# Performance work log

Measured on AMD Instinct MI355X. Metric: run time of the kernel, lower is better.

The kernel has to match this reference:

```python
import jax, jax.numpy as jnp
import numpy as np

ALPHA = 0.2  # LeakyReLU negative slope
NEG_INF = -9e15

def setup_inputs() -> dict:
    key = jax.random.key(0)
    k1, k2, k3, k4, k5 = jax.random.split(key, 5)
    B, N, Fin, Fout = 8, 2048, 128, 128
    h = jax.random.normal(k1, (B, N, Fin), dtype=jnp.float32)
    adj = jax.random.randint(k2, (N, N), 0, 2, dtype=jnp.int32)
    dist = jax.random.uniform(k3, (N, N), dtype=jnp.float32)
    W = jax.random.normal(k4, (Fin, Fout), dtype=jnp.float32) * (1.414 * (6.0 / (Fin + Fout)) ** 0.5)
    a = jax.random.normal(k5, (2 * Fout, 1), dtype=jnp.float32) * 0.1
    distance_scaler = jnp.ones((1,), dtype=jnp.float32)
    return {"h": h, "adj": adj, "dist": dist, "W": W, "a": a, "distance_scaler": distance_scaler}

def reference(h, adj, dist, W, a, distance_scaler):
    # h: [B,N,Fin], adj/dist: [N,N], W: [Fin,Fout], a: [2*Fout,1]
    h_prime = jnp.einsum('bnf,fh->bnh', h, W)              # [B,N,Fout]
    Fout = h_prime.shape[-1]
    a1, a2 = a[:Fout, 0], a[Fout:, 0]
    # additive score: a1.h_i + a2.h_j, equivalent to cat([h_i,h_j]) @ a
    si = h_prime @ a1                                      # [B,N]
    sj = h_prime @ a2                                      # [B,N]
    e = jax.nn.leaky_relu(si[:, :, None] + sj[:, None, :], negative_slope=ALPHA)  # [B,N,N]
    dist_bias = -jnp.log(dist + 1e-6) * distance_scaler[0]  # [N,N]
    scores = e + dist_bias[None, :, :]
    scores = jnp.where(adj[None, :, :] > 0, scores, NEG_INF)
    attention = jax.nn.softmax(scores, axis=2)             # [B,N,N]
    # dropout=identity in eval mode
    out = jnp.einsum('bij,bjh->bih', attention, h_prime)   # [B,N,Fout]
    return jax.nn.elu(out)
```

## Files before the change

kernel.cpp:

```cpp
#include <hip/hip_runtime.h>
#include <hip/hip_bf16.h>

typedef __attribute__((ext_vector_type(4))) float f32x4;
typedef __attribute__((ext_vector_type(8))) short short8;
typedef __attribute__((ext_vector_type(4))) unsigned short ushort4v;
typedef _Float16 f16x8 __attribute__((ext_vector_type(8)));

#define NB 8
#define NN 2048
#define NF 128
#define LOG2E 1.4426950408889634f
#define MASK_NEG_H -60000.0f

static __device__ __forceinline__ unsigned short f2bf(float f) {
    union { __hip_bfloat16 b; unsigned short u; } cv;
    cv.b = __float2bfloat16(f);
    return cv.u;
}

static __device__ __forceinline__ void gload_lds16(const void* g, void* l) {
    __builtin_amdgcn_global_load_lds(
        (const __attribute__((address_space(1))) unsigned int*)g,
        (__attribute__((address_space(3))) unsigned int*)l, 16, 0, 0);
}

__global__ __launch_bounds__(256) void k_pre(
    const float* __restrict__ h, const int* __restrict__ adj,
    const float* __restrict__ dist, const float* __restrict__ W,
    const float* __restrict__ a, const float* __restrict__ scaler,
    unsigned short* __restrict__ vfrag, float* __restrict__ siC,
    float* __restrict__ sjC, _Float16* __restrict__ biasF)
{
    __shared__ __align__(16) unsigned char smem[34816];
    const int bid = blockIdx.x;
    const int t = threadIdx.x;

    if (bid < 256) {
        unsigned char* WT = smem;
        float* wa1 = (float*)(smem + 32768);
        float* wa2 = wa1 + NF;

        const int lane = t & 63;
        const int w = t >> 6;
        const int b = bid >> 5;
        const int i0 = (bid & 31) << 6;

        {
            const int f = t >> 1;
            const int c0 = (t & 1) << 6;
            float s1 = 0.f, s2 = 0.f;
            const float* wrow = W + f * NF + c0;
            const float* a1p = a + c0;
            const float* a2p = a + NF + c0;
            #pragma unroll 8
            for (int c = 0; c < 64; ++c) {
                float wv = wrow[c];
                s1 += wv * a1p[c];
                s2 += wv * a2p[c];
                int col = c0 + c;
                int dst = col * 256 + ((2 * f) ^ ((col & 15) << 4));
                *reinterpret_cast<unsigned short*>(&WT[dst]) = f2bf(wv);
            }
            s1 += __shfl_xor(s1, 1);
            s2 += __shfl_xor(s2, 1);
            if ((t & 1) == 0) { wa1[f] = s1 * LOG2E; wa2[f] = s2 * LOG2E; }
        }
        __syncthreads();

        const int l15 = lane & 15;
        const int arow = i0 + w * 16 + l15;
        const int kofs = (lane >> 4) << 3;
        const float* hrow = h + (size_t)(b * NN + arow) * NF + kofs;
        const int swz = l15 << 4;

        f32x4 acc[8];
        #pragma unroll
        for (int nt = 0; nt < 8; ++nt) acc[nt] = (f32x4)(0.f);
        float s1 = 0.f, s2 = 0.f;

        #pragma unroll
        for (int k0 = 0; k0 < NF; k0 += 32) {
            f32x4 h0 = *reinterpret_cast<const f32x4*>(hrow + k0);
            f32x4 h1 = *reinterpret_cast<const f32x4*>(hrow + k0 + 4);
            f32x4 w1lo = *reinterpret_cast<const f32x4*>(&wa1[k0 + kofs]);
            f32x4 w1hi = *reinterpret_cast<const f32x4*>(&wa1[k0 + kofs + 4]);
            f32x4 w2lo = *reinterpret_cast<const f32x4*>(&wa2[k0 + kofs]);
            f32x4 w2hi = *reinterpret_cast<const f32x4*>(&wa2[k0 + kofs + 4]);
            short8 af;
            #pragma unroll
            for (int e = 0; e < 4; ++e) {
                s1 += h0[e] * w1lo[e] + h1[e] * w1hi[e];
                s2 += h0[e] * w2lo[e] + h1[e] * w2hi[e];
                af[e]     = (short)f2bf(h0[e]);
                af[4 + e] = (short)f2bf(h1[e]);
            }
            const int ib = (2 * (k0 + kofs)) ^ swz;
            #pragma unroll
            for (int nt = 0; nt < 8; ++nt) {
                short8 bf8 = *reinterpret_cast<short8*>(&WT[(nt * 16 + l15) * 256 + ib]);
                acc[nt] = __builtin_amdgcn_mfma_f32_16x16x32_bf16(af, bf8, acc[nt], 0, 0, 0);
            }
        }

        s1 += __shfl_xor(s1, 16); s1 += __shfl_xor(s1, 32);
        s2 += __shfl_xor(s2, 16); s2 += __shfl_xor(s2, 32);
        if (lane < 16) {
            siC[b * NN + arow] = s1;
            sjC[b * NN + arow] = s2;
        }

        const int J0 = i0 + w * 16 + ((lane >> 4) << 2);
        const int s = J0 >> 5;
        const int jq = (J0 >> 3) & 3;
        const int eh = J0 & 7;
        #pragma unroll
        for (int nt = 0; nt < 8; ++nt) {
            ushort4v pk;
            #pragma unroll
            for (int e = 0; e < 4; ++e) pk[e] = f2bf(acc[nt][e]);
            *reinterpret_cast<ushort4v*>(
                vfrag + (((size_t)(b * 64 + s) * 8 + nt) * 64 + (l15 | (jq << 4))) * 8 + eh) = pk;
        }
    } else {
        _Float16 (*st)[64][8] = (_Float16 (*)[64][8])smem;
        const int bid2 = bid - 256;
        const int iblk = bid2 >> 3;
        const int jch = bid2 & 7;
        const int i_l = t >> 4;
        const int o2 = t & 15;
        const int i = iblk * 16 + i_l;
        const int jbase = jch * 256 + o2 * 16;
        const float sc = scaler[0];

        const int* ap = adj + (size_t)i * NN + jbase;
        const float* dp = dist + (size_t)i * NN + jbase;
        int av[16]; float dv[16];
        *reinterpret_cast<int4*>(&av[0])  = *reinterpret_cast<const int4*>(ap);
        *reinterpret_cast<int4*>(&av[4])  = *reinterpret_cast<const int4*>(ap + 4);
        *reinterpret_cast<int4*>(&av[8])  = *reinterpret_cast<const int4*>(ap + 8);
        *reinterpret_cast<int4*>(&av[12]) = *reinterpret_cast<const int4*>(ap + 12);
        *reinterpret_cast<float4*>(&dv[0])  = *reinterpret_cast<const float4*>(dp);
        *reinterpret_cast<float4*>(&dv[4])  = *reinterpret_cast<const float4*>(dp + 4);
        *reinterpret_cast<float4*>(&dv[8])  = *reinterpret_cast<const float4*>(dp + 8);
        *reinterpret_cast<float4*>(&dv[12]) = *reinterpret_cast<const float4*>(dp + 12);

        #pragma unroll
        for (int u = 0; u < 2; ++u) {
            const int sl = (o2 * 2 + u) >> 2;
            const int jq = (o2 * 2 + u) & 3;
            f16x8 pk;
            #pragma unroll
            for (int e = 0; e < 8; ++e) {
                const int idx = u * 8 + e;
                float v = (av[idx] > 0) ? (-__log2f(dv[idx] + 1e-6f) * sc) : MASK_NEG_H;
                pk[e] = (_Float16)v;
            }
            *reinterpret_cast<f16x8*>(&st[sl][i_l | (jq << 4)][0]) = pk;
        }
        __syncthreads();

        const int w = t >> 6, lane = t & 63;
        #pragma unroll
        for (int sub = 0; sub < 2; ++sub) {
            const int fs = w * 2 + sub;
            *reinterpret_cast<f16x8*>(
                biasF + ((size_t)(iblk * 64 + jch * 8 + fs) * 64 + lane) * 8) =
                *reinterpret_cast<f16x8*>(&st[fs][lane][0]);
        }
    }
}

__global__ __launch_bounds__(512) void k_attn(
    const unsigned short* __restrict__ vfrag, const float* __restrict__ siC,
    const float* __restrict__ sjC, const _Float16* __restrict__ biasF,
    float* __restrict__ out)
{
    __shared__ __align__(16) unsigned char vbuf[3][32768];
    __shared__ float lp[2][4][16];

    const int t = threadIdx.x;
    const int lane = t & 63;
    const int w = t >> 6;
    const int rt = w & 3;
    const int jh = w >> 2;
    const int l15 = lane & 15;
    const int hi = lane >> 4;

    const int b = blockIdx.x & 7;
    const int rg = blockIdx.x >> 3;

    const int rowbase = rg * 64 + rt * 16;
    const float si0 = siC[b * NN + rowbase + l15];

    const unsigned short* vsrc = vfrag + (size_t)b * 262144 + w * 512 + lane * 8;
    const int ldst = w * 1024;

    const _Float16* bp = biasF + ((size_t)((rg * 4 + rt) * 64) * 64 + lane) * 8;
    const float* sjb = sjC + b * NN + hi * 8;

    f32x4 acc[8];
    #pragma unroll
    for (int ct = 0; ct < 8; ++ct) acc[ct] = (f32x4)(0.f);
    float ls0 = 0.f;

#define STAGE(TL, BUF)                                                        \
    { const unsigned short* gs = vsrc + (TL) * 16384;                         \
      unsigned char* lb = &vbuf[BUF][ldst];                                   \
      gload_lds16(gs,         lb);                                            \
      gload_lds16(gs + 4096,  lb + 8192);                                     \
      gload_lds16(gs + 8192,  lb + 16384);                                    \
      gload_lds16(gs + 12288, lb + 24576); }

    f32x4 sjA0, sjA1, sjB0, sjB1;
    f16x8 bvA, bvB;

#define PREFETCH_SB(TL)                                                       \
    { const int sA = (TL) * 4 + jh * 2;                                       \
      sjA0 = *reinterpret_cast<const f32x4*>(sjb + sA * 32);                  \
      sjA1 = *reinterpret_cast<const f32x4*>(sjb + sA * 32 + 4);              \
      bvA  = *reinterpret_cast<const f16x8*>(bp + sA * 512);                  \
      sjB0 = *reinterpret_cast<const f32x4*>(sjb + sA * 32 + 32);             \
      sjB1 = *reinterpret_cast<const f32x4*>(sjb + sA * 32 + 36);             \
      bvB  = *reinterpret_cast<const f16x8*>(bp + sA * 512 + 512); }

#define QSTEP(SJ0, SJ1, BV, LSL, BUF)                                         \
    { short8 pa;                                                              \
      _Pragma("unroll")                                                       \
      for (int e = 0; e < 8; ++e) {                                           \
          const float sjv = (e < 4) ? SJ0[e] : SJ1[e - 4];                    \
          float x = si0 + sjv;                                                \
          x = fmaxf(x, 0.2f * x) + (float)BV[e];                              \
          float p = __builtin_amdgcn_exp2f(x);                                \
          ls0 += p;                                                           \
          pa[e] = (short)f2bf(p);                                             \
      }                                                                       \
      _Pragma("unroll")                                                       \
      for (int ct = 0; ct < 8; ++ct) {                                        \
          const short8 bfr = *reinterpret_cast<const short8*>(                \
              &vbuf[BUF][((LSL) * 8 + ct) * 1024 + lane * 16]);               \
          acc[ct] = __builtin_amdgcn_mfma_f32_16x16x32_bf16(pa, bfr, acc[ct], 0, 0, 0); \
      } }

    STAGE(0, 0)
    PREFETCH_SB(0)
    STAGE(1, 1)

    for (int tl = 0; tl < 15; ++tl) {
        const int buf = tl % 3;
        asm volatile("s_waitcnt vmcnt(10)" ::: "memory");
        __builtin_amdgcn_s_barrier();
        QSTEP(sjA0, sjA1, bvA, jh * 2, buf)
        QSTEP(sjB0, sjB1, bvB, jh * 2 + 1, buf)
        PREFETCH_SB(tl + 1)
        if (tl + 2 < 16) STAGE(tl + 2, (tl + 2) % 3)
        __builtin_amdgcn_s_barrier();
    }
    {
        asm volatile("s_waitcnt vmcnt(6)" ::: "memory");
        __builtin_amdgcn_s_barrier();
        QSTEP(sjA0, sjA1, bvA, jh * 2, 0)
        QSTEP(sjB0, sjB1, bvB, jh * 2 + 1, 0)
    }
#undef STAGE
#undef PREFETCH_SB
#undef QSTEP

    ls0 += __shfl_xor(ls0, 16);
    ls0 += __shfl_xor(ls0, 32);
    if (lane < 16) lp[jh][rt][l15] = ls0;
    __syncthreads();

    if (jh == 1) {
        #pragma unroll
        for (int ct = 0; ct < 8; ++ct)
            *reinterpret_cast<f32x4*>(&vbuf[1][(rt * 8 + ct) * 1024 + lane * 16]) = acc[ct];
    }
    __syncthreads();
    if (jh == 0) {
        float linv[4];
        #pragma unroll
        for (int e = 0; e < 4; ++e) {
            const int rr = (hi << 2) + e;
            linv[e] = 1.0f / (lp[0][rt][rr] + lp[1][rt][rr]);
        }
        #pragma unroll
        for (int ct = 0; ct < 8; ++ct) {
            f32x4 o = acc[ct] + *reinterpret_cast<const f32x4*>(
                &vbuf[1][(rt * 8 + ct) * 1024 + lane * 16]);
            const int col = ct * 16 + l15;
            #pragma unroll
            for (int e = 0; e < 4; ++e) {
                const int row = rowbase + (hi << 2) + e;
                float v = o[e] * linv[e];
                v = (v > 0.f) ? v : expm1f(v);
                out[(size_t)(b * NN + row) * NF + col] = v;
            }
        }
    }
}

extern "C" void kernel_launch(void* const* d_in, const int* in_sizes, int n_in,
                              void* d_out, int out_size, void* d_ws, size_t ws_size,
                              hipStream_t stream) {
    (void)in_sizes; (void)n_in; (void)out_size; (void)ws_size;
    const float* h      = (const float*)d_in[0];
    const int*   adj    = (const int*)d_in[1];
    const float* dist   = (const float*)d_in[2];
    const float* W      = (const float*)d_in[3];
    const float* a      = (const float*)d_in[4];
    const float* scaler = (const float*)d_in[5];
    float* out = (float*)d_out;

    char* ws = (char*)d_ws;
    unsigned short* vfrag = (unsigned short*)ws;
    float* siC      = (float*)(ws + 4 * 1024 * 1024);
    float* sjC      = (float*)(ws + 4 * 1024 * 1024 + 65536);
    _Float16* biasF = (_Float16*)(ws + 4 * 1024 * 1024 + 2 * 65536);

    k_pre<<<dim3(1280), dim3(256), 0, stream>>>(h, adj, dist, W, a, scaler,
                                                vfrag, siC, sjC, biasF);
    k_attn<<<dim3(NB * NN / 64), dim3(512), 0, stream>>>(vfrag, siC, sjC, biasF, out);
}
```

Measured before the change: 43.45 us.

## Deepen attention pipeline to four smaller stages and stage bias through LDS

The j-loop now runs as 32 half-size tiles in a 4-deep LDS ring instead of 16 tiles in a 3-deep ring. Each stage loads V and the fp16 bias tile into LDS with async global-to-LDS loads, so bias no longer goes through per-thread register prefetches. The loop also drops one barrier per iteration, and the MFMA section is wrapped in s_setprio to favour matrix issue. The intent is more loads in flight and less exposed memory latency, at the cost of more, smaller iterations with a barrier each and a changed LDS footprint for the final reduction.

```diff
diff --git a/kernel.cpp b/kernel.cpp
--- a/kernel.cpp
+++ b/kernel.cpp
@@ -175,7 +175,7 @@
     const float* __restrict__ sjC, const _Float16* __restrict__ biasF,
     float* __restrict__ out)
 {
-    __shared__ __align__(16) unsigned char vbuf[3][32768];
+    __shared__ __align__(16) unsigned char vbuf[4][24576];
     __shared__ float lp[2][4][16];
 
     const int t = threadIdx.x;
@@ -192,77 +192,75 @@
     const int rowbase = rg * 64 + rt * 16;
     const float si0 = siC[b * NN + rowbase + l15];
 
-    const unsigned short* vsrc = vfrag + (size_t)b * 262144 + w * 512 + lane * 8;
-    const int ldst = w * 1024;
-
-    const _Float16* bp = biasF + ((size_t)((rg * 4 + rt) * 64) * 64 + lane) * 8;
     const float* sjb = sjC + b * NN + hi * 8;
+    const unsigned short* vsrcb = vfrag + (size_t)b * 262144 + w * 512 + lane * 8;
+    const _Float16* bsrcb = biasF + ((size_t)((rg * 4 + (w & 3)) * 64) * 64 + lane) * 8;
 
     f32x4 acc[8];
     #pragma unroll
     for (int ct = 0; ct < 8; ++ct) acc[ct] = (f32x4)(0.f);
     float ls0 = 0.f;
-
-#define STAGE(TL, BUF)                                                        \
-    { const unsigned short* gs = vsrc + (TL) * 16384;                         \
-      unsigned char* lb = &vbuf[BUF][ldst];                                   \
-      gload_lds16(gs,         lb);                                            \
-      gload_lds16(gs + 4096,  lb + 8192);                                     \
-      gload_lds16(gs + 8192,  lb + 16384);                                    \
-      gload_lds16(gs + 12288, lb + 24576); }
-
-    f32x4 sjA0, sjA1, sjB0, sjB1;
-    f16x8 bvA, bvB;
-
-#define PREFETCH_SB(TL)                                                       \
-    { const int sA = (TL) * 4 + jh * 2;                                       \
+    f32x4 sjA0, sjA1;
+
+#define STAGE(TL)                                                             \
+    { unsigned char* lb = &vbuf[(TL) & 3][w * 1024];                          \
+      const unsigned short* gsV = vsrcb + (TL) * 8192;                        \
+      gload_lds16(gsV,        lb);                                            \
+      gload_lds16(gsV + 4096, lb + 8192);                                     \
+      gload_lds16(bsrcb + (size_t)(2 * (TL) + (w >> 2)) * 512,                \
+                  &vbuf[(TL) & 3][16384 + w * 1024]); }
+
+#define PF_SJ(TL)                                                             \
+    { const int sA = 2 * (TL) + jh;                                           \
       sjA0 = *reinterpret_cast<const f32x4*>(sjb + sA * 32);                  \
-      sjA1 = *reinterpret_cast<const f32x4*>(sjb + sA * 32 + 4);              \
-      bvA  = *reinterpret_cast<const f16x8*>(bp + sA * 512);                  \
-      sjB0 = *reinterpret_cast<const f32x4*>(sjb + sA * 32 + 32);             \
-      sjB1 = *reinterpret_cast<const f32x4*>(sjb + sA * 32 + 36);             \
-      bvB  = *reinterpret_cast<const f16x8*>(bp + sA * 512 + 512); }
-
-#define QSTEP(SJ0, SJ1, BV, LSL, BUF)                                         \
-    { short8 pa;                                                              \
+      sjA1 = *reinterpret_cast<const f32x4*>(sjb + sA * 32 + 4); }
+
+#define QSTEP(BUF)                                                            \
+    { const f16x8 bv = *reinterpret_cast<const f16x8*>(                       \
+          &vbuf[BUF][16384 + (jh * 4 + rt) * 1024 + lane * 16]);              \
+      short8 pa;                                                              \
       _Pragma("unroll")                                                       \
       for (int e = 0; e < 8; ++e) {                                           \
-          const float sjv = (e < 4) ? SJ0[e] : SJ1[e - 4];                    \
+          const float sjv = (e < 4) ? sjA0[e] : sjA1[e - 4];                  \
           float x = si0 + sjv;                                                \
-          x = fmaxf(x, 0.2f * x) + (float)BV[e];                              \
+          x = fmaxf(x, 0.2f * x) + (float)bv[e];                              \
           float p = __builtin_amdgcn_exp2f(x);                                \
           ls0 += p;                                                           \
           pa[e] = (short)f2bf(p);                                             \
       }                                                                       \
+      __builtin_amdgcn_s_setprio(1);                                          \
       _Pragma("unroll")                                                       \
       for (int ct = 0; ct < 8; ++ct) {                                        \
           const short8 bfr = *reinterpret_cast<const short8*>(                \
-              &vbuf[BUF][((LSL) * 8 + ct) * 1024 + lane * 16]);               \
+              &vbuf[BUF][jh * 8192 + ct * 1024 + lane * 16]);                 \
           acc[ct] = __builtin_amdgcn_mfma_f32_16x16x32_bf16(pa, bfr, acc[ct], 0, 0, 0); \
-      } }
-
-    STAGE(0, 0)
-    PREFETCH_SB(0)
-    STAGE(1, 1)
-
-    for (int tl = 0; tl < 15; ++tl) {
-        const int buf = tl % 3;
-        asm volatile("s_waitcnt vmcnt(10)" ::: "memory");
+      }                                                                       \
+      __builtin_amdgcn_s_setprio(0); }
+
+    STAGE(0)
+    PF_SJ(0)
+    asm volatile("" ::: "memory");
+    STAGE(1)
+    STAGE(2)
+
+    for (int tl = 0; tl < 30; ++tl) {
+        asm volatile("s_waitcnt vmcnt(3)" ::: "memory");
         __builtin_amdgcn_s_barrier();
-        QSTEP(sjA0, sjA1, bvA, jh * 2, buf)
-        QSTEP(sjB0, sjB1, bvB, jh * 2 + 1, buf)
-        PREFETCH_SB(tl + 1)
-        if (tl + 2 < 16) STAGE(tl + 2, (tl + 2) % 3)
-        __builtin_amdgcn_s_barrier();
+        QSTEP(tl & 3)
+        PF_SJ(tl + 1)
+        asm volatile("" ::: "memory");
+        if (tl < 29) STAGE(tl + 3)
     }
-    {
-        asm volatile("s_waitcnt vmcnt(6)" ::: "memory");
-        __builtin_amdgcn_s_barrier();
-        QSTEP(sjA0, sjA1, bvA, jh * 2, 0)
-        QSTEP(sjB0, sjB1, bvB, jh * 2 + 1, 0)
-    }
+    asm volatile("s_waitcnt vmcnt(3)" ::: "memory");
+    __builtin_amdgcn_s_barrier();
+    QSTEP(2)
+    PF_SJ(31)
+    asm volatile("s_waitcnt vmcnt(0)" ::: "memory");
+    __builtin_amdgcn_s_barrier();
+    QSTEP(3)
+
 #undef STAGE
-#undef PREFETCH_SB
+#undef PF_SJ
 #undef QSTEP
 
     ls0 += __shfl_xor(ls0, 16);
@@ -273,7 +271,9 @@
     if (jh == 1) {
         #pragma unroll
         for (int ct = 0; ct < 8; ++ct)
-            *reinterpret_cast<f32x4*>(&vbuf[1][(rt * 8 + ct) * 1024 + lane * 16]) = acc[ct];
+            *reinterpret_cast<f32x4*>(
+                &vbuf[0][((rt * 8 + ct) * 64 + lane) * 16 % 24576 +
+                         (((rt * 8 + ct) * 64 + lane) * 16 / 24576) * 24576]) = acc[ct];
     }
     __syncthreads();
     if (jh == 0) {
@@ -285,8 +285,9 @@
         }
         #pragma unroll
         for (int ct = 0; ct < 8; ++ct) {
+            const int off = ((rt * 8 + ct) * 64 + lane) * 16;
             f32x4 o = acc[ct] + *reinterpret_cast<const f32x4*>(
-                &vbuf[1][(rt * 8 + ct) * 1024 + lane * 16]);
+                &vbuf[0][off % 24576 + (off / 24576) * 24576]);
             const int col = ct * 16 + l15;
             #pragma unroll
             for (int e = 0; e < 4; ++e) {
```

After: 49.52 us. +14.0%, slower.

## Factor exponentials out of attention scores and drop the per-tile trailing barrier

Applied to the files above, without the earlier changes.

Rewrites exp2(leaky(si+sj)+bias) as max(2^si*2^sj, 2^(0.2si)*2^(0.2sj)) * 2^bias, so the exponentials are computed once per node and once per adjacency entry in the prep kernel. The inner loop then needs only multiplies and a max instead of an exp per score. The bias is stored as a bf16 multiplier, with zero for masked edges. It also removes the second barrier per tile, raises wave priority around the MFMA section, and adjusts the vmcnt waits. The risks are overflow or underflow of the factored exponentials, since there is no max subtraction, and a possible LDS race now that the trailing barrier is gone.

```diff
diff --git a/kernel.cpp b/kernel.cpp
--- a/kernel.cpp
+++ b/kernel.cpp
@@ -3,19 +3,22 @@
 
 typedef __attribute__((ext_vector_type(4))) float f32x4;
 typedef __attribute__((ext_vector_type(8))) short short8;
+typedef __attribute__((ext_vector_type(8))) unsigned short ushort8;
 typedef __attribute__((ext_vector_type(4))) unsigned short ushort4v;
-typedef _Float16 f16x8 __attribute__((ext_vector_type(8)));
 
 #define NB 8
 #define NN 2048
 #define NF 128
 #define LOG2E 1.4426950408889634f
-#define MASK_NEG_H -60000.0f
 
 static __device__ __forceinline__ unsigned short f2bf(float f) {
     union { __hip_bfloat16 b; unsigned short u; } cv;
     cv.b = __float2bfloat16(f);
     return cv.u;
+}
+
+static __device__ __forceinline__ float bf2f(unsigned short u) {
+    return __uint_as_float(((unsigned int)u) << 16);
 }
 
 static __device__ __forceinline__ void gload_lds16(const void* g, void* l) {
@@ -29,7 +32,8 @@
     const float* __restrict__ dist, const float* __restrict__ W,
     const float* __restrict__ a, const float* __restrict__ scaler,
     unsigned short* __restrict__ vfrag, float* __restrict__ siC,
-    float* __restrict__ sjC, _Float16* __restrict__ biasF)
+    float* __restrict__ EJ, float* __restrict__ FJ,
+    unsigned short* __restrict__ biasF)
 {
     __shared__ __align__(16) unsigned char smem[34816];
     const int bid = blockIdx.x;
@@ -106,7 +110,8 @@
         s2 += __shfl_xor(s2, 16); s2 += __shfl_xor(s2, 32);
         if (lane < 16) {
             siC[b * NN + arow] = s1;
-            sjC[b * NN + arow] = s2;
+            EJ[b * NN + arow] = __builtin_amdgcn_exp2f(s2);
+            FJ[b * NN + arow] = __builtin_amdgcn_exp2f(0.2f * s2);
         }
 
         const int J0 = i0 + w * 16 + ((lane >> 4) << 2);
@@ -122,7 +127,7 @@
                 vfrag + (((size_t)(b * 64 + s) * 8 + nt) * 64 + (l15 | (jq << 4))) * 8 + eh) = pk;
         }
     } else {
-        _Float16 (*st)[64][8] = (_Float16 (*)[64][8])smem;
+        unsigned short (*st)[64][8] = (unsigned short (*)[64][8])smem;
         const int bid2 = bid - 256;
         const int iblk = bid2 >> 3;
         const int jch = bid2 & 7;
@@ -148,14 +153,16 @@
         for (int u = 0; u < 2; ++u) {
             const int sl = (o2 * 2 + u) >> 2;
             const int jq = (o2 * 2 + u) & 3;
-            f16x8 pk;
+            ushort8 pk;
             #pragma unroll
             for (int e = 0; e < 8; ++e) {
                 const int idx = u * 8 + e;
-                float v = (av[idx] > 0) ? (-__log2f(dv[idx] + 1e-6f) * sc) : MASK_NEG_H;
-                pk[e] = (_Float16)v;
-            }
-            *reinterpret_cast<f16x8*>(&st[sl][i_l | (jq << 4)][0]) = pk;
+                float v = (av[idx] > 0)
+                    ? __builtin_amdgcn_exp2f(-__log2f(dv[idx] + 1e-6f) * sc)
+                    : 0.0f;
+                pk[e] = f2bf(v);
+            }
+            *reinterpret_cast<ushort8*>(&st[sl][i_l | (jq << 4)][0]) = pk;
         }
         __syncthreads();
 
@@ -163,17 +170,17 @@
         #pragma unroll
         for (int sub = 0; sub < 2; ++sub) {
             const int fs = w * 2 + sub;
-            *reinterpret_cast<f16x8*>(
+            *reinterpret_cast<ushort8*>(
                 biasF + ((size_t)(iblk * 64 + jch * 8 + fs) * 64 + lane) * 8) =
-                *reinterpret_cast<f16x8*>(&st[fs][lane][0]);
+                *reinterpret_cast<ushort8*>(&st[fs][lane][0]);
         }
     }
 }
 
 __global__ __launch_bounds__(512) void k_attn(
     const unsigned short* __restrict__ vfrag, const float* __restrict__ siC,
-    const float* __restrict__ sjC, const _Float16* __restrict__ biasF,
-    float* __restrict__ out)
+    const float* __restrict__ EJ, const float* __restrict__ FJ,
+    const unsigned short* __restrict__ biasF, float* __restrict__ out)
 {
     __shared__ __align__(16) unsigned char vbuf[3][32768];
     __shared__ float lp[2][4][16];
@@ -190,13 +197,16 @@
     const int rg = blockIdx.x >> 3;
 
     const int rowbase = rg * 64 + rt * 16;
-    const float si0 = siC[b * NN + rowbase + l15];
+    const float si_v = siC[b * NN + rowbase + l15];
+    const float e_i = __builtin_amdgcn_exp2f(si_v);
+    const float f_i = __builtin_amdgcn_exp2f(0.2f * si_v);
 
     const unsigned short* vsrc = vfrag + (size_t)b * 262144 + w * 512 + lane * 8;
     const int ldst = w * 1024;
 
-    const _Float16* bp = biasF + ((size_t)((rg * 4 + rt) * 64) * 64 + lane) * 8;
-    const float* sjb = sjC + b * NN + hi * 8;
+    const unsigned short* bp = biasF + ((size_t)((rg * 4 + rt) * 64) * 64 + lane) * 8;
+    const float* ejb = EJ + b * NN + hi * 8;
+    const float* fjb = FJ + b * NN + hi * 8;
 
     f32x4 acc[8];
     #pragma unroll
@@ -211,56 +221,61 @@
       gload_lds16(gs + 8192,  lb + 16384);                                    \
       gload_lds16(gs + 12288, lb + 24576); }
 
-    f32x4 sjA0, sjA1, sjB0, sjB1;
-    f16x8 bvA, bvB;
+    f32x4 ejA0, ejA1, fjA0, fjA1, ejB0, ejB1, fjB0, fjB1;
+    ushort8 bvA, bvB;
 
 #define PREFETCH_SB(TL)                                                       \
     { const int sA = (TL) * 4 + jh * 2;                                       \
-      sjA0 = *reinterpret_cast<const f32x4*>(sjb + sA * 32);                  \
-      sjA1 = *reinterpret_cast<const f32x4*>(sjb + sA * 32 + 4);              \
-      bvA  = *reinterpret_cast<const f16x8*>(bp + sA * 512);                  \
-      sjB0 = *reinterpret_cast<const f32x4*>(sjb + sA * 32 + 32);             \
-      sjB1 = *reinterpret_cast<const f32x4*>(sjb + sA * 32 + 36);             \
-      bvB  = *reinterpret_cast<const f16x8*>(bp + sA * 512 + 512); }
-
-#define QSTEP(SJ0, SJ1, BV, LSL, BUF)                                         \
+      ejA0 = *reinterpret_cast<const f32x4*>(ejb + sA * 32);                  \
+      ejA1 = *reinterpret_cast<const f32x4*>(ejb + sA * 32 + 4);              \
+      fjA0 = *reinterpret_cast<const f32x4*>(fjb + sA * 32);                  \
+      fjA1 = *reinterpret_cast<const f32x4*>(fjb + sA * 32 + 4);              \
+      bvA  = *reinterpret_cast<const ushort8*>(bp + sA * 512);                \
+      ejB0 = *reinterpret_cast<const f32x4*>(ejb + sA * 32 + 32);             \
+      ejB1 = *reinterpret_cast<const f32x4*>(ejb + sA * 32 + 36);             \
+      fjB0 = *reinterpret_cast<const f32x4*>(fjb + sA * 32 + 32);             \
+      fjB1 = *reinterpret_cast<const f32x4*>(fjb + sA * 32 + 36);             \
+      bvB  = *reinterpret_cast<const ushort8*>(bp + sA * 512 + 512); }
+
+#define QSTEP(EJ0, EJ1, FJ0, FJ1, BV, LSL, BUF)                               \
     { short8 pa;                                                              \
       _Pragma("unroll")                                                       \
       for (int e = 0; e < 8; ++e) {                                           \
-          const float sjv = (e < 4) ? SJ0[e] : SJ1[e - 4];                    \
-          float x = si0 + sjv;                                                \
-          x = fmaxf(x, 0.2f * x) + (float)BV[e];                              \
-          float p = __builtin_amdgcn_exp2f(x);                                \
+          const float ej = (e < 4) ? EJ0[e] : EJ1[e - 4];                     \
+          const float fj = (e < 4) ? FJ0[e] : FJ1[e - 4];                     \
+          float p = fmaxf(e_i * ej, f_i * fj) * bf2f(BV[e]);                  \
           ls0 += p;                                                           \
           pa[e] = (short)f2bf(p);                                             \
       }                                                                       \
+      __builtin_amdgcn_s_setprio(1);                                          \
       _Pragma("unroll")                                                       \
       for (int ct = 0; ct < 8; ++ct) {                                        \
           const short8 bfr = *reinterpret_cast<const short8*>(                \
               &vbuf[BUF][((LSL) * 8 + ct) * 1024 + lane * 16]);               \
           acc[ct] = __builtin_amdgcn_mfma_f32_16x16x32_bf16(pa, bfr, acc[ct], 0, 0, 0); \
-      } }
+      }                                                                       \
+      __builtin_amdgcn_s_setprio(0); }
 
     STAGE(0, 0)
     PREFETCH_SB(0)
+    asm volatile("" ::: "memory");
     STAGE(1, 1)
 
     for (int tl = 0; tl < 15; ++tl) {
         const int buf = tl % 3;
-        asm volatile("s_waitcnt vmcnt(10)" ::: "memory");
+        asm volatile("s_waitcnt vmcnt(14)" ::: "memory");
         __builtin_amdgcn_s_barrier();
-        QSTEP(sjA0, sjA1, bvA, jh * 2, buf)
-        QSTEP(sjB0, sjB1, bvB, jh * 2 + 1, buf)
+        QSTEP(ejA0, ejA1, fjA0, fjA1, bvA, jh * 2, buf)
+        QSTEP(ejB0, ejB1, fjB0, fjB1, bvB, jh * 2 + 1, buf)
         PREFETCH_SB(tl + 1)
-        if (tl + 2 < 16) STAGE(tl + 2, (tl + 2) % 3)
-        __builtin_amdgcn_s_barrier();
+        asm volatile("" ::: "memory");
+        if (tl < 14) STAGE(tl + 2, (tl + 2) % 3)
     }
-    {
-        asm volatile("s_waitcnt vmcnt(6)" ::: "memory");
-        __builtin_amdgcn_s_barrier();
-        QSTEP(sjA0, sjA1, bvA, jh * 2, 0)
-        QSTEP(sjB0, sjB1, bvB, jh * 2 + 1, 0)
-    }
+    asm volatile("s_waitcnt vmcnt(10)" ::: "memory");
+    __builtin_amdgcn_s_barrier();
+    QSTEP(ejA0, ejA1, fjA0, fjA1, bvA, jh * 2, 0)
+    QSTEP(ejB0, ejB1, fjB0, fjB1, bvB, jh * 2 + 1, 0)
+
 #undef STAGE
 #undef PREFETCH_SB
 #undef QSTEP
@@ -314,10 +329,12 @@
     char* ws = (char*)d_ws;
     unsigned short* vfrag = (unsigned short*)ws;
     float* siC      = (float*)(ws + 4 * 1024 * 1024);
-    float* sjC      = (float*)(ws + 4 * 1024 * 1024 + 65536);
-    _Float16* biasF = (_Float16*)(ws + 4 * 1024 * 1024 + 2 * 65536);
+    float* EJ       = (float*)(ws + 4 * 1024 * 1024 + 65536);
+    float* FJ       = (float*)(ws + 4 * 1024 * 1024 + 2 * 65536);
+    unsigned short* biasF =
+        (unsigned short*)(ws + 4 * 1024 * 1024 + 3 * 65536);
 
     k_pre<<<dim3(1280), dim3(256), 0, stream>>>(h, adj, dist, W, a, scaler,
-                                                vfrag, siC, sjC, biasF);
-    k_attn<<<dim3(NB * NN / 64), dim3(512), 0, stream>>>(vfrag, siC, sjC, biasF, out);
-}
+                                                vfrag, siC, EJ, FJ, biasF);
+    k_attn<<<dim3(NB * NN / 64), dim3(512), 0, stream>>>(vfrag, siC, EJ, FJ, biasF, out);
+}
```

Measured after the change: 50.86 us. +17.1%, slower.
